# Kernel optimization log

Measured on AMD Instinct MI355X. Metric: run time of the kernel, lower is better.

The kernel has to match this reference:

```python
import jax, jax.numpy as jnp
import numpy as np

N_CODEBOOKS = 9
CODEBOOK_SIZE = 1024
CODEBOOK_DIM = 8
INPUT_DIM = 128
B, T = 16, 4096


def setup_inputs() -> dict:
    key = jax.random.key(0)
    ks = jax.random.split(key, 7)
    x = jax.random.normal(ks[0], (B, 2 * INPUT_DIM, T), dtype=jnp.float32)
    noise = jax.random.normal(ks[1], (B, INPUT_DIM, T), dtype=jnp.float32)
    # per-codebook params (stacked over the quantizer axis)
    in_w = jax.random.normal(ks[2], (N_CODEBOOKS, CODEBOOK_DIM, INPUT_DIM), dtype=jnp.float32) * 0.08
    in_b = jax.random.normal(ks[3], (N_CODEBOOKS, CODEBOOK_DIM), dtype=jnp.float32) * 0.01
    codebook = jax.random.normal(ks[4], (N_CODEBOOKS, CODEBOOK_SIZE, CODEBOOK_DIM), dtype=jnp.float32)
    out_w = jax.random.normal(ks[5], (N_CODEBOOKS, INPUT_DIM, CODEBOOK_DIM), dtype=jnp.float32) * 0.08
    out_b = jax.random.normal(ks[6], (N_CODEBOOKS, INPUT_DIM), dtype=jnp.float32) * 0.01
    return {"x": x, "noise": noise, "in_w": in_w, "in_b": in_b,
            "codebook": codebook, "out_w": out_w, "out_b": out_b}


def _l2norm(v, eps=1e-12):
    n = jnp.linalg.norm(v, axis=-1, keepdims=True)
    return v / jnp.maximum(n, eps)


def reference(x, noise, in_w, in_b, codebook, out_w, out_b):
    # --- vae_sample ---
    mean, scale = jnp.split(x, 2, axis=1)
    stdev = jax.nn.softplus(scale) + 1e-4
    var = stdev * stdev
    kl = jnp.mean(jnp.sum(mean * mean + var - jnp.log(var) - 1.0, axis=1))
    z = noise * stdev + mean  # [B, D, T]

    # --- ResidualVectorQuantize (eval mode, all codebooks) ---
    residual = z
    z_q = jnp.zeros_like(z)
    commitment_loss = jnp.float32(0.0)
    codebook_loss = jnp.float32(0.0)
    codes, lats = [], []
    b, _, t = z.shape
    for i in range(N_CODEBOOKS):
        # in_proj (1x1 conv)
        z_e = jnp.einsum("cd,bdt->bct", in_w[i], residual) + in_b[i][None, :, None]
        enc = z_e.transpose(0, 2, 1).reshape(b * t, CODEBOOK_DIM)
        enc_n = _l2norm(enc)
        cb_n = _l2norm(codebook[i])
        # squared L2 distance between normalized vectors
        dist = (jnp.sum(enc_n * enc_n, axis=1, keepdims=True)
                - 2.0 * enc_n @ cb_n.T
                + jnp.sum(cb_n * cb_n, axis=1)[None, :])
        idx = jnp.argmin(dist, axis=1).reshape(b, t)  # [B, T]
        zq_i = codebook[i][idx].transpose(0, 2, 1)  # [B, c, T] (raw codebook)
        # mse_loss(...).mean([1,2]).mean() == global mean
        commitment_loss = commitment_loss + jnp.mean((z_e - jax.lax.stop_gradient(zq_i)) ** 2)
        codebook_loss = codebook_loss + jnp.mean((zq_i - jax.lax.stop_gradient(z_e)) ** 2)
        # straight-through estimator
        zq_st = z_e + jax.lax.stop_gradient(zq_i - z_e)
        out = jnp.einsum("dc,bct->bdt", out_w[i], zq_st) + out_b[i][None, :, None]
        z_q = z_q + out
        residual = residual - out
        codes.append(idx)
        lats.append(z_e)
    codes = jnp.stack(codes, axis=1)          # [B, N, T]
    latents = jnp.concatenate(lats, axis=1)   # [B, N*c, T]
    commitment_loss = commitment_loss / N_CODEBOOKS
    codebook_loss = codebook_loss / N_CODEBOOKS
    return z_q, kl, commitment_loss, codebook_loss, codes, latents
```

## Files before the change

kernel.cpp:

```cpp
#include <hip/hip_runtime.h>
#include <cstdint>
#include <cstddef>

constexpr int T   = 4096;
constexpr int BB  = 16;
constexpr int D   = 128;
constexpr int CB  = 1024;
constexpr int CD  = 8;
constexpr int NCB = 9;

constexpr int TBLK = 64;
constexpr int NTHR = 256;
constexpr int ZLS  = 66;

constexpr size_t OFF_ZQ    = 0;
constexpr size_t OFF_SCAL  = (size_t)BB * D * T;
constexpr size_t OFF_CODES = OFF_SCAL + 3;
constexpr size_t OFF_LAT   = OFF_CODES + (size_t)BB * NCB * T;

constexpr size_t AFR_U32 = (size_t)NCB * 64 * 2 * 64 * 4;
constexpr size_t H2C_F32 = (size_t)NCB * CB;
constexpr size_t AFW_U32 = (size_t)2 * 6 * 2 * 5 * 64 * 4;
constexpr size_t CM_F32  = (size_t)NCB * 72 * 8;
constexpr size_t OBS_F32 = 128;
constexpr size_t BEF_F32 = 72;
constexpr size_t OP_F32  = (size_t)NCB * CB * D;

typedef short bf16x8 __attribute__((ext_vector_type(8)));
typedef float f32x4  __attribute__((ext_vector_type(4)));

__device__ __forceinline__ unsigned short f2bf(float f) {
    unsigned u = __float_as_uint(f);
    return (unsigned short)((u + (((u >> 16) & 1u) + 0x7FFFu)) >> 16);
}
__device__ __forceinline__ float bf2f(unsigned short b) {
    return __uint_as_float((unsigned)b << 16);
}

constexpr int PAIR_A[6] = {0, 0, 1, 1, 2, 0};
constexpr int PAIR_B[6] = {0, 1, 0, 1, 0, 2};

__device__ __forceinline__ unsigned short splitterm(float xv, int term) {
    unsigned short t0 = f2bf(xv); if (term == 0) return t0;
    float r1 = xv - bf2f(t0);
    unsigned short t1 = f2bf(r1); if (term == 1) return t1;
    float r2 = r1 - bf2f(t1);
    return f2bf(r2);
}

__global__ void prep_kernel(const float* __restrict__ codebook,
                            const float* __restrict__ in_w,
                            const float* __restrict__ in_b,
                            const float* __restrict__ out_w,
                            const float* __restrict__ out_b,
                            unsigned* __restrict__ afr,
                            float* __restrict__ h2c,
                            unsigned* __restrict__ afw,
                            float* __restrict__ CMt,
                            float* __restrict__ obs,
                            float* __restrict__ bef,
                            float* __restrict__ OPt,
                            float* __restrict__ scal) {
    const int gid = blockIdx.x * blockDim.x + threadIdx.x;
    if (gid == 0) { scal[0] = 0.f; scal[1] = 0.f; scal[2] = 0.f; }

    if (gid < NCB * CB) {
        const int e  = gid;
        const int i  = e >> 10;
        const int en = e & 1023;
        const int et = en >> 4;
        const int m  = en & 15;

        float v[CD]; float s2 = 0.f;
#pragma unroll
        for (int j = 0; j < CD; ++j) { v[j] = codebook[(size_t)e * CD + j]; s2 = fmaf(v[j], v[j], s2); }
        float inv = 1.0f / fmaxf(sqrtf(s2), 1e-12f);
        float cn[CD]; float c2 = 0.f;
#pragma unroll
        for (int j = 0; j < CD; ++j) { cn[j] = v[j] * inv; c2 = fmaf(cn[j], cn[j], c2); }
        h2c[e] = -0.5f * c2;

        unsigned pk[3][4];
#pragma unroll
        for (int w = 0; w < 4; ++w) {
            float x0 = cn[2 * w], x1 = cn[2 * w + 1];
            unsigned short a0 = f2bf(x0); float r0 = x0 - bf2f(a0);
            unsigned short a1 = f2bf(r0); float q0 = r0 - bf2f(a1);
            unsigned short a2 = f2bf(q0);
            unsigned short b0 = f2bf(x1); float r1 = x1 - bf2f(b0);
            unsigned short b1 = f2bf(r1); float q1 = r1 - bf2f(b1);
            unsigned short b2 = f2bf(q1);
            pk[0][w] = (unsigned)a0 | ((unsigned)b0 << 16);
            pk[1][w] = (unsigned)a1 | ((unsigned)b1 << 16);
            pk[2][w] = (unsigned)a2 | ((unsigned)b2 << 16);
        }
        const int At[8] = {0, 1, 2, 0, 1, 0, 2, 1};
#pragma unroll
        for (int kh = 0; kh < 2; ++kh) {
#pragma unroll
            for (int h = 0; h < 4; ++h) {
                int A1 = At[kh * 4 + (h >> 1)];
                int A2 = At[kh * 4 + 2 + (h >> 1)];
                int dw = (h & 1) * 2;
                size_t off = ((((size_t)i * 64 + et) * 2 + kh) * 64 + (h * 16 + m)) * 4;
                afr[off + 0] = pk[A1][dw];
                afr[off + 1] = pk[A1][dw + 1];
                afr[off + 2] = pk[A2][dw];
                afr[off + 3] = pk[A2][dw + 1];
            }
        }
        return;
    }
    if (gid < 2 * NCB * CB) {
        const int e = gid - NCB * CB;
        const int i = e >> 10;
        float cv[CD];
#pragma unroll
        for (int d = 0; d < CD; ++d) cv[d] = codebook[(size_t)e * CD + d];
        const float* ow = out_w + (size_t)i * D * CD;
        float* dst = OPt + (size_t)e * D;
        for (int r = 0; r < D; ++r) {
            float a = 0.f;
#pragma unroll
            for (int d = 0; d < CD; ++d) a = fmaf(ow[r * CD + d], cv[d], a);
            dst[r] = a;
        }
        return;
    }
    if (gid < 2 * NCB * CB + NCB * 72) {
        const int idx = gid - 2 * NCB * CB;
        const int j = idx / 72, r = idx - j * 72;
        const float* wi = in_w + (size_t)r * D;
        const float* ow = out_w + (size_t)j * D * CD;
        float a[CD];
#pragma unroll
        for (int d = 0; d < CD; ++d) a[d] = 0.f;
        for (int k = 0; k < D; ++k) {
            float w = wi[k];
#pragma unroll
            for (int d = 0; d < CD; ++d) a[d] = fmaf(w, ow[k * CD + d], a[d]);
        }
#pragma unroll
        for (int d = 0; d < CD; ++d) CMt[((size_t)j * 72 + r) * CD + d] = a[d];
        return;
    }
    if (gid < 2 * NCB * CB + NCB * 72 + 128) {
        const int r = gid - (2 * NCB * CB + NCB * 72);
        float a = 0.f;
        for (int i = 0; i < NCB; ++i) a += out_b[(size_t)i * D + r];
        obs[r] = a;
        return;
    }
    if (gid < 2 * NCB * CB + NCB * 72 + 128 + 72) {
        const int row = gid - (2 * NCB * CB + NCB * 72 + 128);
        const int ic  = row >> 3;
        const float* wi = in_w + (size_t)row * D;
        float a = in_b[row];
        for (int j = 0; j < ic; ++j) {
            const float* ob = out_b + (size_t)j * D;
            float s = 0.f;
            for (int k = 0; k < D; ++k) s = fmaf(wi[k], ob[k], s);
            a -= s;
        }
        bef[row] = a;
        return;
    }
    if (gid < 2 * NCB * CB + NCB * 72 + 128 + 72 + 7680) {
        int idx = gid - (2 * NCB * CB + NCB * 72 + 128 + 72);
        const int lane = idx & 63; idx >>= 6;
        const int mt = idx % 5; idx /= 5;
        const int kq = idx & 1; idx >>= 1;
        const int p  = idx % 6;
        const int P  = idx / 6;
        const int h  = lane >> 4, m = lane & 15;
        const int row = mt * 16 + m;
        const int term = PAIR_A[p];
        const int D0 = P * 64 + kq * 32 + h * 4;
        const int doff[4][2] = {{0, 1}, {2, 3}, {16, 17}, {18, 19}};
        unsigned wv[4];
#pragma unroll
        for (int w = 0; w < 4; ++w) {
            unsigned short lo = 0, hi = 0;
            if (row < 72) {
                lo = splitterm(in_w[(size_t)row * D + D0 + doff[w][0]], term);
                hi = splitterm(in_w[(size_t)row * D + D0 + doff[w][1]], term);
            }
            wv[w] = (unsigned)lo | ((unsigned)hi << 16);
        }
        *reinterpret_cast<uint4*>(afw + ((size_t)(((P * 6 + p) * 2 + kq) * 5 + mt) * 64 + lane) * 4)
            = make_uint4(wv[0], wv[1], wv[2], wv[3]);
        return;
    }
}

__global__ __launch_bounds__(NTHR, 4)
void rvq_kernel(const float* __restrict__ x,
                const float* __restrict__ noise,
                const float* __restrict__ codebook,
                const unsigned* __restrict__ afr,
                const float* __restrict__ h2c,
                const unsigned* __restrict__ afw,
                const float* __restrict__ CMt,
                const float* __restrict__ obs,
                const float* __restrict__ bef,
                const float* __restrict__ OPt,
                float* __restrict__ o_zq,
                float* __restrict__ o_scal,
                float* __restrict__ o_codes,
                float* __restrict__ o_lat) {
    __shared__ char     zbuf[24576];
    __shared__ unsigned es[TBLK * 12];
    __shared__ float    redS[4 * TBLK];
    __shared__ int      redI[4 * TBLK];
    __shared__ int      cidx[NCB * TBLK];
    __shared__ float    redw[8];

    uint2* zs = reinterpret_cast<uint2*>(zbuf);
    float* Zl = reinterpret_cast<float*>(zbuf);

    const int tid = threadIdx.x;
    const int c   = tid & 63;
    const int s   = tid >> 6;
    const int su  = __builtin_amdgcn_readfirstlane(s);
    const int b   = blockIdx.x >> 6;
    const int t0  = (blockIdx.x & 63) << 6;
    const int t   = t0 + c;

    const int l  = tid & 63;
    const int h  = l >> 4;
    const int nl = l & 15;

    float kl_local = 0.f;
    f32x4 acc[5];
#pragma unroll
    for (int mt = 0; mt < 5; ++mt) {
        int row0 = mt * 16 + h * 4;
        if (row0 < 72) acc[mt] = *reinterpret_cast<const f32x4*>(bef + row0);
        else           acc[mt] = f32x4{0.f, 0.f, 0.f, 0.f};
    }

#pragma unroll 1
    for (int P = 0; P < 2; ++P) {
        {
            const int r0 = P * 64 + su * 16;
            const float* xm = x     + (size_t)b * 2 * D * T + (size_t)r0 * T + t;
            const float* xs = xm    + (size_t)D * T;
            const float* nz = noise + (size_t)b * D * T     + (size_t)r0 * T + t;
            float zrow[16];
#pragma unroll
            for (int k = 0; k < 16; ++k) {
                float m  = xm[(size_t)k * T];
                float sc = xs[(size_t)k * T];
                float nv = nz[(size_t)k * T];
                float sp  = fmaxf(sc, 0.f) + log1pf(expf(-fabsf(sc)));
                float sd  = sp + 1e-4f;
                float var = sd * sd;
                zrow[k]   = fmaf(nv, sd, m);
                kl_local += m * m + var - logf(var) - 1.0f;
            }
#pragma unroll
            for (int db = 0; db < 4; ++db) {
                unsigned w[3][2];
#pragma unroll
                for (int half = 0; half < 2; ++half) {
                    float x0 = zrow[db * 4 + half * 2], x1 = zrow[db * 4 + half * 2 + 1];
                    unsigned short a0 = f2bf(x0); float r1 = x0 - bf2f(a0);
                    unsigned short a1 = f2bf(r1); float r2 = r1 - bf2f(a1);
                    unsigned short a2 = f2bf(r2);
                    unsigned short b0 = f2bf(x1); float s1v = x1 - bf2f(b0);
                    unsigned short b1 = f2bf(s1v); float s2v = s1v - bf2f(b1);
                    unsigned short b2 = f2bf(s2v);
                    w[0][half] = (unsigned)a0 | ((unsigned)b0 << 16);
                    w[1][half] = (unsigned)a1 | ((unsigned)b1 << 16);
                    w[2][half] = (unsigned)a2 | ((unsigned)b2 << 16);
                }
#pragma unroll
                for (int tt = 0; tt < 3; ++tt)
                    zs[(tt * 16 + su * 4 + db) * 64 + c] = make_uint2(w[tt][0], w[tt][1]);
            }
        }
        __syncthreads();
        {
            const int colB = su * 16 + nl;
#pragma unroll
            for (int p = 0; p < 6; ++p) {
#pragma unroll
                for (int kq = 0; kq < 2; ++kq) {
                    uint2 blo = zs[(PAIR_B[p] * 16 + kq * 8 + h) * 64 + colB];
                    uint2 bhi = zs[(PAIR_B[p] * 16 + kq * 8 + 4 + h) * 64 + colB];
                    uint4 bu = make_uint4(blo.x, blo.y, bhi.x, bhi.y);
                    bf16x8 bfr = *reinterpret_cast<bf16x8*>(&bu);
                    const uint4* Aw = reinterpret_cast<const uint4*>(afw)
                                      + (size_t)(((P * 6 + p) * 2 + kq) * 5) * 64 + l;
#pragma unroll
                    for (int mt = 0; mt < 5; ++mt) {
                        uint4 au = Aw[(size_t)mt * 64];
                        bf16x8 af = *reinterpret_cast<bf16x8*>(&au);
                        acc[mt] = __builtin_amdgcn_mfma_f32_16x16x32_bf16(af, bfr, acc[mt], 0, 0, 0);
                    }
                }
            }
        }
        __syncthreads();
    }
#pragma unroll
    for (int mt = 0; mt < 5; ++mt)
#pragma unroll
        for (int r = 0; r < 4; ++r)
            Zl[(mt * 16 + h * 4 + r) * ZLS + su * 16 + nl] = acc[mt][r];

    float loss_local = 0.f;

    for (int i = 0; i < NCB; ++i) {
        __syncthreads();

        if (tid < 64) {
            float v[CD]; float n2 = 0.f;
#pragma unroll
            for (int j = 0; j < CD; ++j) { v[j] = Zl[(i * CD + j) * ZLS + tid]; n2 = fmaf(v[j], v[j], n2); }
            float inv = 1.0f / fmaxf(sqrtf(n2), 1e-12f);
            unsigned pk[3][4];
#pragma unroll
            for (int w = 0; w < 4; ++w) {
                float x0 = v[2 * w] * inv, x1 = v[2 * w + 1] * inv;
                unsigned short a0 = f2bf(x0); float r0 = x0 - bf2f(a0);
                unsigned short a1 = f2bf(r0); float q0 = r0 - bf2f(a1);
                unsigned short a2 = f2bf(q0);
                unsigned short b0 = f2bf(x1); float r1 = x1 - bf2f(b0);
                unsigned short b1 = f2bf(r1); float q1 = r1 - bf2f(b1);
                unsigned short b2 = f2bf(q1);
                pk[0][w] = (unsigned)a0 | ((unsigned)b0 << 16);
                pk[1][w] = (unsigned)a1 | ((unsigned)b1 << 16);
                pk[2][w] = (unsigned)a2 | ((unsigned)b2 << 16);
            }
            uint4* ep = reinterpret_cast<uint4*>(&es[(size_t)tid * 12]);
            ep[0] = make_uint4(pk[0][0], pk[0][1], pk[0][2], pk[0][3]);
            ep[1] = make_uint4(pk[1][0], pk[1][1], pk[1][2], pk[1][3]);
            ep[2] = make_uint4(pk[2][0], pk[2][1], pk[2][2], pk[2][3]);
        }
        {
            float la0 = Zl[(i * CD + su) * ZLS + c];
            float la1 = Zl[(i * CD + su + 4) * ZLS + c];
            o_lat[(size_t)b * (NCB * CD) * T + (size_t)(i * CD + su) * T + t]     = la0;
            o_lat[(size_t)b * (NCB * CD) * T + (size_t)(i * CD + su + 4) * T + t] = la1;
        }
        __syncthreads();

        bf16x8 bfrag[4][2];
        {
            const int dwo = (h & 1) * 2;
            const int tA  = h >> 1;
            const int tB  = 1 + (h >> 1);
#pragma unroll
            for (int pt = 0; pt < 4; ++pt) {
                const int col = pt * 16 + nl;
                uint2 lo0 = *reinterpret_cast<const uint2*>(&es[col * 12 + 0 * 4 + dwo]);
                uint2 hi0 = *reinterpret_cast<const uint2*>(&es[col * 12 + tA * 4 + dwo]);
                uint2 lh1 = *reinterpret_cast<const uint2*>(&es[col * 12 + tB * 4 + dwo]);
                uint4 t0v = make_uint4(lo0.x, lo0.y, hi0.x, hi0.y);
                uint4 t1v = make_uint4(lh1.x, lh1.y, lh1.x, lh1.y);
                bfrag[pt][0] = *reinterpret_cast<bf16x8*>(&t0v);
                bfrag[pt][1] = *reinterpret_cast<bf16x8*>(&t1v);
            }
        }

        float best[4] = {-3.0e38f, -3.0e38f, -3.0e38f, -3.0e38f};
        int   bidx[4] = {0, 0, 0, 0};
        {
            const uint4* Ab = reinterpret_cast<const uint4*>(afr)
                              + ((size_t)(i * 64 + su * 16) * 2) * 64 + l;
            const f32x4* Hb = reinterpret_cast<const f32x4*>(h2c + (size_t)i * CB + su * 256);
            int eb = (su * 16) * 16 + h * 4;
#pragma unroll 2
            for (int e16 = 0; e16 < 16; ++e16) {
                uint4 ua0 = Ab[0];
                uint4 ua1 = Ab[64];
                f32x4 hv  = Hb[e16 * 4 + h];
                bf16x8 a0 = *reinterpret_cast<bf16x8*>(&ua0);
                bf16x8 a1 = *reinterpret_cast<bf16x8*>(&ua1);
#pragma unroll
                for (int pt = 0; pt < 4; ++pt) {
                    f32x4 accd = __builtin_amdgcn_mfma_f32_16x16x32_bf16(a0, bfrag[pt][0], hv, 0, 0, 0);
                    accd = __builtin_amdgcn_mfma_f32_16x16x32_bf16(a1, bfrag[pt][1], accd, 0, 0, 0);
#pragma unroll
                    for (int r = 0; r < 4; ++r) {
                        float sc = accd[r];
                        if (sc > best[pt]) { best[pt] = sc; bidx[pt] = eb + r; }
                    }
                }
                Ab += 128; eb += 16;
            }
        }

#pragma unroll
        for (int off = 16; off <= 32; off <<= 1) {
#pragma unroll
            for (int pt = 0; pt < 4; ++pt) {
                float ob = __shfl_xor(best[pt], off, 64);
                int   oi = __shfl_xor(bidx[pt], off, 64);
                bool tk = (ob > best[pt]) || (ob == best[pt] && oi < bidx[pt]);
                if (tk) { best[pt] = ob; bidx[pt] = oi; }
            }
        }
        if (l < 16) {
#pragma unroll
            for (int pt = 0; pt < 4; ++pt) {
                redS[su * 64 + pt * 16 + l] = best[pt];
                redI[su * 64 + pt * 16 + l] = bidx[pt];
            }
        }
        __syncthreads();

        float bsc = redS[c];
        int   bi  = redI[c];
#pragma unroll
        for (int ww = 1; ww < 4; ++ww) {
            float v2 = redS[ww * TBLK + c];
            int   vi = redI[ww * TBLK + c];
            if (v2 > bsc) { bsc = v2; bi = vi; }
        }
        cidx[i * TBLK + c] = bi;
        if (s == 0) o_codes[(size_t)b * NCB * T + (size_t)i * T + t] = (float)bi;

        float cv[CD];
        {
            const float4* cr4 = (const float4*)(codebook + ((size_t)i * CB + bi) * CD);
            float4 qa = cr4[0], qb = cr4[1];
            cv[0] = qa.x; cv[1] = qa.y; cv[2] = qa.z; cv[3] = qa.w;
            cv[4] = qb.x; cv[5] = qb.y; cv[6] = qb.z; cv[7] = qb.w;
            if (s == 0) {
#pragma unroll
                for (int j = 0; j < CD; ++j) {
                    float dd = cv[j] - Zl[(i * CD + j) * ZLS + c];
                    loss_local = fmaf(dd, dd, loss_local);
                }
            }
        }

        {
            const int nf = 64 - 8 * i;
            for (int rr = su; rr < nf; rr += 4) {
                const int row = (i + 1) * 8 + rr;
                float zv = Zl[row * ZLS + c];
                const float* cm = CMt + ((size_t)i * 72 + row) * CD;
#pragma unroll
                for (int d2 = 0; d2 < CD; ++d2) zv = fmaf(-cm[d2], cv[d2], zv);
                Zl[row * ZLS + c] = zv;
            }
        }
    }
    __syncthreads();

    {
        f32x4 oa[8];
#pragma unroll
        for (int kb = 0; kb < 8; ++kb)
            oa[kb] = *reinterpret_cast<const f32x4*>(obs + su * 32 + kb * 4);
#pragma unroll
        for (int i2 = 0; i2 < NCB; ++i2) {
            int code = cidx[i2 * TBLK + c];
            const f32x4* op = reinterpret_cast<const f32x4*>(OPt + ((size_t)(i2 * CB + code)) * D + su * 32);
#pragma unroll
            for (int kb = 0; kb < 8; ++kb) oa[kb] += op[kb];
        }
        float* oq = o_zq + (size_t)b * D * T + (size_t)(su * 32) * T + t;
#pragma unroll
        for (int kb = 0; kb < 8; ++kb)
#pragma unroll
            for (int r = 0; r < 4; ++r)
                oq[(size_t)(kb * 4 + r) * T] = oa[kb][r];
    }

    float v = kl_local;
#pragma unroll
    for (int o = 32; o > 0; o >>= 1) v += __shfl_down(v, o, 64);
    float w2 = loss_local;
#pragma unroll
    for (int o = 32; o > 0; o >>= 1) w2 += __shfl_down(w2, o, 64);
    if ((tid & 63) == 0) { redw[s] = v; redw[4 + s] = w2; }
    __syncthreads();
    if (tid == 0) {
        float ks = redw[0] + redw[1] + redw[2] + redw[3];
        float ls = redw[4] + redw[5] + redw[6] + redw[7];
        atomicAdd(&o_scal[0], ks * (1.0f / 65536.0f));
        float lsn = ls * (1.0f / (524288.0f * 9.0f));
        atomicAdd(&o_scal[1], lsn);
        atomicAdd(&o_scal[2], lsn);
    }
}

extern "C" void kernel_launch(void* const* d_in, const int* in_sizes, int n_in,
                              void* d_out, int out_size, void* d_ws, size_t ws_size,
                              hipStream_t stream) {
    const float* x        = (const float*)d_in[0];
    const float* noise    = (const float*)d_in[1];
    const float* in_w     = (const float*)d_in[2];
    const float* in_b     = (const float*)d_in[3];
    const float* codebook = (const float*)d_in[4];
    const float* out_w    = (const float*)d_in[5];
    const float* out_b    = (const float*)d_in[6];

    float* out     = (float*)d_out;
    float* o_zq    = out + OFF_ZQ;
    float* o_scal  = out + OFF_SCAL;
    float* o_codes = out + OFF_CODES;
    float* o_lat   = out + OFF_LAT;

    unsigned* afr = (unsigned*)d_ws;
    float*    h2c = (float*)(afr + AFR_U32);
    unsigned* afw = (unsigned*)(h2c + H2C_F32);
    float*    CMt = (float*)(afw + AFW_U32);
    float*    obs = CMt + CM_F32;
    float*    bef = obs + OBS_F32;
    float*    OPt = bef + BEF_F32;

    const int prep_total = 2 * NCB * CB + NCB * 72 + 128 + 72 + 7680;
    prep_kernel<<<(prep_total + 255) / 256, 256, 0, stream>>>(
        codebook, in_w, in_b, out_w, out_b, afr, h2c, afw, CMt, obs, bef, OPt, o_scal);

    dim3 grid(BB * (T / TBLK));
    rvq_kernel<<<grid, NTHR, 0, stream>>>(x, noise, codebook,
                                          afr, h2c, afw, CMt, obs, bef, OPt,
                                          o_zq, o_scal, o_codes, o_lat);
}
```

Measured before the change: 389.0 us.

## Split RVQ block work across eight waves instead of four

Doubles the threads per block from 256 to 512 and repartitions every phase across eight wavefronts: the VAE sampling rows, the in-projection MFMA tiles (split 3/2 across wave halves), the codebook search (128 codes per wave), the residual update rows and the output accumulation. The aim is more parallelism and latency hiding per 64-timestep tile, with fewer serial iterations per wave. The cost is more barrier participants, uneven MFMA tile splits, and higher register and occupancy pressure under the new launch bounds.

```diff
diff --git a/kernel.cpp b/kernel.cpp
--- a/kernel.cpp
+++ b/kernel.cpp
@@ -10,7 +10,8 @@
 constexpr int NCB = 9;
 
 constexpr int TBLK = 64;
-constexpr int NTHR = 256;
+constexpr int NTHR = 512;
+constexpr int NW   = 8;
 constexpr int ZLS  = 66;
 
 constexpr size_t OFF_ZQ    = 0;
@@ -193,7 +194,7 @@
     }
 }
 
-__global__ __launch_bounds__(NTHR, 4)
+__global__ __launch_bounds__(NTHR, 8)
 void rvq_kernel(const float* __restrict__ x,
                 const float* __restrict__ noise,
                 const float* __restrict__ codebook,
@@ -210,10 +211,10 @@
                 float* __restrict__ o_lat) {
     __shared__ char     zbuf[24576];
     __shared__ unsigned es[TBLK * 12];
-    __shared__ float    redS[4 * TBLK];
-    __shared__ int      redI[4 * TBLK];
+    __shared__ float    redS[NW * TBLK];
+    __shared__ int      redI[NW * TBLK];
     __shared__ int      cidx[NCB * TBLK];
-    __shared__ float    redw[8];
+    __shared__ float    redw[2 * NW];
 
     uint2* zs = reinterpret_cast<uint2*>(zbuf);
     float* Zl = reinterpret_cast<float*>(zbuf);
@@ -230,25 +231,27 @@
     const int h  = l >> 4;
     const int nl = l & 15;
 
+    const int mtbase = (su < 4) ? 0 : 3;
+    const int nmt    = (su < 4) ? 3 : 2;
     float kl_local = 0.f;
-    f32x4 acc[5];
-#pragma unroll
-    for (int mt = 0; mt < 5; ++mt) {
-        int row0 = mt * 16 + h * 4;
-        if (row0 < 72) acc[mt] = *reinterpret_cast<const f32x4*>(bef + row0);
-        else           acc[mt] = f32x4{0.f, 0.f, 0.f, 0.f};
+    f32x4 acc[3];
+#pragma unroll
+    for (int q = 0; q < 3; ++q) {
+        int row0 = (mtbase + q) * 16 + h * 4;
+        if (q < nmt && row0 < 72) acc[q] = *reinterpret_cast<const f32x4*>(bef + row0);
+        else                      acc[q] = f32x4{0.f, 0.f, 0.f, 0.f};
     }
 
 #pragma unroll 1
     for (int P = 0; P < 2; ++P) {
         {
-            const int r0 = P * 64 + su * 16;
+            const int r0 = P * 64 + su * 8;
             const float* xm = x     + (size_t)b * 2 * D * T + (size_t)r0 * T + t;
             const float* xs = xm    + (size_t)D * T;
             const float* nz = noise + (size_t)b * D * T     + (size_t)r0 * T + t;
-            float zrow[16];
-#pragma unroll
-            for (int k = 0; k < 16; ++k) {
+            float zrow[8];
+#pragma unroll
+            for (int k = 0; k < 8; ++k) {
                 float m  = xm[(size_t)k * T];
                 float sc = xs[(size_t)k * T];
                 float nv = nz[(size_t)k * T];
@@ -259,7 +262,7 @@
                 kl_local += m * m + var - logf(var) - 1.0f;
             }
 #pragma unroll
-            for (int db = 0; db < 4; ++db) {
+            for (int db = 0; db < 2; ++db) {
                 unsigned w[3][2];
 #pragma unroll
                 for (int half = 0; half < 2; ++half) {
@@ -276,12 +279,12 @@
                 }
 #pragma unroll
                 for (int tt = 0; tt < 3; ++tt)
-                    zs[(tt * 16 + su * 4 + db) * 64 + c] = make_uint2(w[tt][0], w[tt][1]);
+                    zs[(tt * 16 + su * 2 + db) * 64 + c] = make_uint2(w[tt][0], w[tt][1]);
             }
         }
         __syncthreads();
         {
-            const int colB = su * 16 + nl;
+            const int colB = (su & 3) * 16 + nl;
 #pragma unroll
             for (int p = 0; p < 6; ++p) {
 #pragma unroll
@@ -293,10 +296,12 @@
                     const uint4* Aw = reinterpret_cast<const uint4*>(afw)
                                       + (size_t)(((P * 6 + p) * 2 + kq) * 5) * 64 + l;
 #pragma unroll
-                    for (int mt = 0; mt < 5; ++mt) {
-                        uint4 au = Aw[(size_t)mt * 64];
-                        bf16x8 af = *reinterpret_cast<bf16x8*>(&au);
-                        acc[mt] = __builtin_amdgcn_mfma_f32_16x16x32_bf16(af, bfr, acc[mt], 0, 0, 0);
+                    for (int q = 0; q < 3; ++q) {
+                        if (q < nmt) {
+                            uint4 au = Aw[(size_t)(mtbase + q) * 64];
+                            bf16x8 af = *reinterpret_cast<bf16x8*>(&au);
+                            acc[q] = __builtin_amdgcn_mfma_f32_16x16x32_bf16(af, bfr, acc[q], 0, 0, 0);
+                        }
                     }
                 }
             }
@@ -304,10 +309,13 @@
         __syncthreads();
     }
 #pragma unroll
-    for (int mt = 0; mt < 5; ++mt)
-#pragma unroll
-        for (int r = 0; r < 4; ++r)
-            Zl[(mt * 16 + h * 4 + r) * ZLS + su * 16 + nl] = acc[mt][r];
+    for (int q = 0; q < 3; ++q) {
+        if (q < nmt) {
+#pragma unroll
+            for (int r = 0; r < 4; ++r)
+                Zl[((mtbase + q) * 16 + h * 4 + r) * ZLS + (su & 3) * 16 + nl] = acc[q][r];
+        }
+    }
 
     float loss_local = 0.f;
 
@@ -339,10 +347,8 @@
             ep[2] = make_uint4(pk[2][0], pk[2][1], pk[2][2], pk[2][3]);
         }
         {
-            float la0 = Zl[(i * CD + su) * ZLS + c];
-            float la1 = Zl[(i * CD + su + 4) * ZLS + c];
-            o_lat[(size_t)b * (NCB * CD) * T + (size_t)(i * CD + su) * T + t]     = la0;
-            o_lat[(size_t)b * (NCB * CD) * T + (size_t)(i * CD + su + 4) * T + t] = la1;
+            float la = Zl[(i * CD + su) * ZLS + c];
+            o_lat[(size_t)b * (NCB * CD) * T + (size_t)(i * CD + su) * T + t] = la;
         }
         __syncthreads();
 
@@ -368,14 +374,15 @@
         int   bidx[4] = {0, 0, 0, 0};
         {
             const uint4* Ab = reinterpret_cast<const uint4*>(afr)
-                              + ((size_t)(i * 64 + su * 16) * 2) * 64 + l;
-            const f32x4* Hb = reinterpret_cast<const f32x4*>(h2c + (size_t)i * CB + su * 256);
-            int eb = (su * 16) * 16 + h * 4;
+                              + ((size_t)(i * 64 + su * 8) * 2) * 64 + l;
+            const f32x4* Hb = reinterpret_cast<const f32x4*>(h2c)
+                              + (size_t)i * 256 + su * 32;
+            int eb = su * 128 + h * 4;
 #pragma unroll 2
-            for (int e16 = 0; e16 < 16; ++e16) {
+            for (int e8 = 0; e8 < 8; ++e8) {
                 uint4 ua0 = Ab[0];
                 uint4 ua1 = Ab[64];
-                f32x4 hv  = Hb[e16 * 4 + h];
+                f32x4 hv  = Hb[e8 * 4 + h];
                 bf16x8 a0 = *reinterpret_cast<bf16x8*>(&ua0);
                 bf16x8 a1 = *reinterpret_cast<bf16x8*>(&ua1);
 #pragma unroll
@@ -414,7 +421,7 @@
         float bsc = redS[c];
         int   bi  = redI[c];
 #pragma unroll
-        for (int ww = 1; ww < 4; ++ww) {
+        for (int ww = 1; ww < NW; ++ww) {
             float v2 = redS[ww * TBLK + c];
             int   vi = redI[ww * TBLK + c];
             if (v2 > bsc) { bsc = v2; bi = vi; }
@@ -439,7 +446,7 @@
 
         {
             const int nf = 64 - 8 * i;
-            for (int rr = su; rr < nf; rr += 4) {
+            for (int rr = su; rr < nf; rr += NW) {
                 const int row = (i + 1) * 8 + rr;
                 float zv = Zl[row * ZLS + c];
                 const float* cm = CMt + ((size_t)i * 72 + row) * CD;
@@ -452,20 +459,20 @@
     __syncthreads();
 
     {
-        f32x4 oa[8];
-#pragma unroll
-        for (int kb = 0; kb < 8; ++kb)
-            oa[kb] = *reinterpret_cast<const f32x4*>(obs + su * 32 + kb * 4);
+        f32x4 oa[4];
+#pragma unroll
+        for (int kb = 0; kb < 4; ++kb)
+            oa[kb] = *reinterpret_cast<const f32x4*>(obs + su * 16 + kb * 4);
 #pragma unroll
         for (int i2 = 0; i2 < NCB; ++i2) {
             int code = cidx[i2 * TBLK + c];
-            const f32x4* op = reinterpret_cast<const f32x4*>(OPt + ((size_t)(i2 * CB + code)) * D + su * 32);
-#pragma unroll
-            for (int kb = 0; kb < 8; ++kb) oa[kb] += op[kb];
-        }
-        float* oq = o_zq + (size_t)b * D * T + (size_t)(su * 32) * T + t;
-#pragma unroll
-        for (int kb = 0; kb < 8; ++kb)
+            const f32x4* op = reinterpret_cast<const f32x4*>(OPt + ((size_t)(i2 * CB + code)) * D + su * 16);
+#pragma unroll
+            for (int kb = 0; kb < 4; ++kb) oa[kb] += op[kb];
+        }
+        float* oq = o_zq + (size_t)b * D * T + (size_t)(su * 16) * T + t;
+#pragma unroll
+        for (int kb = 0; kb < 4; ++kb)
 #pragma unroll
             for (int r = 0; r < 4; ++r)
                 oq[(size_t)(kb * 4 + r) * T] = oa[kb][r];
@@ -477,11 +484,12 @@
     float w2 = loss_local;
 #pragma unroll
     for (int o = 32; o > 0; o >>= 1) w2 += __shfl_down(w2, o, 64);
-    if ((tid & 63) == 0) { redw[s] = v; redw[4 + s] = w2; }
+    if ((tid & 63) == 0) { redw[s] = v; redw[NW + s] = w2; }
     __syncthreads();
     if (tid == 0) {
-        float ks = redw[0] + redw[1] + redw[2] + redw[3];
-        float ls = redw[4] + redw[5] + redw[6] + redw[7];
+        float ks = 0.f, ls = 0.f;
+#pragma unroll
+        for (int q = 0; q < NW; ++q) { ks += redw[q]; ls += redw[NW + q]; }
         atomicAdd(&o_scal[0], ks * (1.0f / 65536.0f));
         float lsn = ls * (1.0f / (524288.0f * 9.0f));
         atomicAdd(&o_scal[1], lsn);
```

Result: slower. 800.0 us (+105.7%).

## Raise occupancy via shared-memory aliasing and dual-chain argmax MFMA loop

Applied to the files above, without the earlier changes.

Raises launch bounds from 4 to 6 blocks per CU and aliases the reduction and encoding scratch buffers into the unused tail of the z buffer to cut LDS per block. Skips writing padded accumulator rows past 72 so that tail stays free. Restructures the codebook-search loop to run two independent MFMA chains with separate running argmax state and merge them at the end, exposing more ILP. The higher occupancy target constrains register use and may cause spills, especially with the doubled best/index state.

```diff
diff --git a/kernel.cpp b/kernel.cpp
--- a/kernel.cpp
+++ b/kernel.cpp
@@ -193,7 +193,7 @@
     }
 }
 
-__global__ __launch_bounds__(NTHR, 4)
+__global__ __launch_bounds__(NTHR, 6)
 void rvq_kernel(const float* __restrict__ x,
                 const float* __restrict__ noise,
                 const float* __restrict__ codebook,
@@ -208,15 +208,15 @@
                 float* __restrict__ o_scal,
                 float* __restrict__ o_codes,
                 float* __restrict__ o_lat) {
-    __shared__ char     zbuf[24576];
-    __shared__ unsigned es[TBLK * 12];
-    __shared__ float    redS[4 * TBLK];
-    __shared__ int      redI[4 * TBLK];
-    __shared__ int      cidx[NCB * TBLK];
-    __shared__ float    redw[8];
-
-    uint2* zs = reinterpret_cast<uint2*>(zbuf);
-    float* Zl = reinterpret_cast<float*>(zbuf);
+    __shared__ char  zbuf[24576];
+    __shared__ int   cidx[NCB * TBLK];
+    __shared__ float redw[8];
+
+    uint2*    zs   = reinterpret_cast<uint2*>(zbuf);
+    float*    Zl   = reinterpret_cast<float*>(zbuf);
+    float*    redS = reinterpret_cast<float*>(zbuf + 19008);
+    int*      redI = reinterpret_cast<int*>(zbuf + 20032);
+    unsigned* es   = reinterpret_cast<unsigned*>(zbuf + 21504);
 
     const int tid = threadIdx.x;
     const int c   = tid & 63;
@@ -304,10 +304,14 @@
         __syncthreads();
     }
 #pragma unroll
-    for (int mt = 0; mt < 5; ++mt)
-#pragma unroll
-        for (int r = 0; r < 4; ++r)
-            Zl[(mt * 16 + h * 4 + r) * ZLS + su * 16 + nl] = acc[mt][r];
+    for (int mt = 0; mt < 5; ++mt) {
+        const int row0 = mt * 16 + h * 4;
+        if (row0 < 72) {
+#pragma unroll
+            for (int r = 0; r < 4; ++r)
+                Zl[(row0 + r) * ZLS + su * 16 + nl] = acc[mt][r];
+        }
+    }
 
     float loss_local = 0.f;
 
@@ -364,49 +368,66 @@
             }
         }
 
-        float best[4] = {-3.0e38f, -3.0e38f, -3.0e38f, -3.0e38f};
-        int   bidx[4] = {0, 0, 0, 0};
+        float best0[4] = {-3.0e38f, -3.0e38f, -3.0e38f, -3.0e38f};
+        float best1[4] = {-3.0e38f, -3.0e38f, -3.0e38f, -3.0e38f};
+        int   bidx0[4] = {0, 0, 0, 0};
+        int   bidx1[4] = {0, 0, 0, 0};
         {
             const uint4* Ab = reinterpret_cast<const uint4*>(afr)
                               + ((size_t)(i * 64 + su * 16) * 2) * 64 + l;
             const f32x4* Hb = reinterpret_cast<const f32x4*>(h2c + (size_t)i * CB + su * 256);
-            int eb = (su * 16) * 16 + h * 4;
+            int eb = su * 256 + h * 4;
 #pragma unroll 2
-            for (int e16 = 0; e16 < 16; ++e16) {
-                uint4 ua0 = Ab[0];
-                uint4 ua1 = Ab[64];
-                f32x4 hv  = Hb[e16 * 4 + h];
-                bf16x8 a0 = *reinterpret_cast<bf16x8*>(&ua0);
-                bf16x8 a1 = *reinterpret_cast<bf16x8*>(&ua1);
+            for (int ep2 = 0; ep2 < 8; ++ep2) {
+                uint4 uaa0 = Ab[0];
+                uint4 uaa1 = Ab[64];
+                uint4 uba0 = Ab[128];
+                uint4 uba1 = Ab[192];
+                f32x4 hva  = Hb[(2 * ep2) * 4 + h];
+                f32x4 hvb  = Hb[(2 * ep2 + 1) * 4 + h];
+                bf16x8 aa0 = *reinterpret_cast<bf16x8*>(&uaa0);
+                bf16x8 aa1 = *reinterpret_cast<bf16x8*>(&uaa1);
+                bf16x8 ba0 = *reinterpret_cast<bf16x8*>(&uba0);
+                bf16x8 ba1 = *reinterpret_cast<bf16x8*>(&uba1);
 #pragma unroll
                 for (int pt = 0; pt < 4; ++pt) {
-                    f32x4 accd = __builtin_amdgcn_mfma_f32_16x16x32_bf16(a0, bfrag[pt][0], hv, 0, 0, 0);
-                    accd = __builtin_amdgcn_mfma_f32_16x16x32_bf16(a1, bfrag[pt][1], accd, 0, 0, 0);
+                    f32x4 accA = __builtin_amdgcn_mfma_f32_16x16x32_bf16(aa0, bfrag[pt][0], hva, 0, 0, 0);
+                    accA = __builtin_amdgcn_mfma_f32_16x16x32_bf16(aa1, bfrag[pt][1], accA, 0, 0, 0);
+                    f32x4 accB = __builtin_amdgcn_mfma_f32_16x16x32_bf16(ba0, bfrag[pt][0], hvb, 0, 0, 0);
+                    accB = __builtin_amdgcn_mfma_f32_16x16x32_bf16(ba1, bfrag[pt][1], accB, 0, 0, 0);
 #pragma unroll
                     for (int r = 0; r < 4; ++r) {
-                        float sc = accd[r];
-                        if (sc > best[pt]) { best[pt] = sc; bidx[pt] = eb + r; }
+                        float scA = accA[r];
+                        if (scA > best0[pt]) { best0[pt] = scA; bidx0[pt] = eb + r; }
+                        float scB = accB[r];
+                        if (scB > best1[pt]) { best1[pt] = scB; bidx1[pt] = eb + 16 + r; }
                     }
                 }
-                Ab += 128; eb += 16;
-            }
+                Ab += 256; eb += 32;
+            }
+        }
+#pragma unroll
+        for (int pt = 0; pt < 4; ++pt) {
+            bool tk = (best1[pt] > best0[pt]) ||
+                      (best1[pt] == best0[pt] && bidx1[pt] < bidx0[pt]);
+            if (tk) { best0[pt] = best1[pt]; bidx0[pt] = bidx1[pt]; }
         }
 
 #pragma unroll
         for (int off = 16; off <= 32; off <<= 1) {
 #pragma unroll
             for (int pt = 0; pt < 4; ++pt) {
-                float ob = __shfl_xor(best[pt], off, 64);
-                int   oi = __shfl_xor(bidx[pt], off, 64);
-                bool tk = (ob > best[pt]) || (ob == best[pt] && oi < bidx[pt]);
-                if (tk) { best[pt] = ob; bidx[pt] = oi; }
+                float ob = __shfl_xor(best0[pt], off, 64);
+                int   oi = __shfl_xor(bidx0[pt], off, 64);
+                bool tk = (ob > best0[pt]) || (ob == best0[pt] && oi < bidx0[pt]);
+                if (tk) { best0[pt] = ob; bidx0[pt] = oi; }
             }
         }
         if (l < 16) {
 #pragma unroll
             for (int pt = 0; pt < 4; ++pt) {
-                redS[su * 64 + pt * 16 + l] = best[pt];
-                redI[su * 64 + pt * 16 + l] = bidx[pt];
+                redS[su * 64 + pt * 16 + l] = best0[pt];
+                redI[su * 64 + pt * 16 + l] = bidx0[pt];
             }
         }
         __syncthreads();
```

Result: slower. 707.3 us (+81.8%).
